# Kernel tuning notes

Hardware: AMD Instinct MI355X
Metric: run time of the kernel (lower is better)

## Reference

```python
import jax, jax.numpy as jnp
import numpy as np

B, T = 64, 4096
CAT_COLS = [0, 1, 2, 3]
VOCABS = [1000, 5000, 200, 50]
EMB_DIMS = [32, 64, 16, 8]
NUM_COLS = list(range(4, 12))  # 8 numeric columns


def setup_inputs() -> dict:
    key = jax.random.key(0)
    ks = jax.random.split(key, 16)
    # numeric part of the dataset
    num = jax.random.normal(ks[0], (B, T, len(NUM_COLS)), dtype=jnp.float32)
    # categorical columns hold raw category ids stored as floats (as in the torch dataset)
    cats = [jax.random.randint(ks[1 + i], (B, T, 1), 0, v).astype(jnp.float32)
            for i, v in enumerate(VOCABS)]
    dataset = jnp.concatenate(cats + [num], axis=-1)  # [B, T, 12]
    inp = {"dataset": dataset}
    for i, (v, d) in enumerate(zip(VOCABS, EMB_DIMS)):
        inp[f"emb{i}"] = jax.random.normal(ks[8 + i], (v, d), dtype=jnp.float32) * 0.02
        # mapping dict {raw_value: contiguous_idx} materialized as a lookup table;
        # unique values are 0..v-1 so the table is the identity permutation
        inp[f"lut{i}"] = jnp.arange(v, dtype=jnp.int32)
    return inp


def reference(dataset, emb0, emb1, emb2, emb3, lut0, lut1, lut2, lut3):
    embs = [emb0, emb1, emb2, emb3]
    luts = [lut0, lut1, lut2, lut3]
    feats = []
    for col, lut, tab in zip(CAT_COLS, luts, embs):
        raw = dataset[:, :, col].astype(jnp.int32)      # [B, T] raw category ids
        mapped = lut[raw]                               # dict remap -> contiguous ids
        feats.append(tab[mapped])                       # [B, T, emb_dim] embedding gather
    feats.append(dataset[:, :, NUM_COLS[0]:NUM_COLS[-1] + 1])  # numeric features [B, T, 8]
    out = jnp.concatenate(feats, axis=-1)               # [B, T, 128]
    return out.reshape(dataset.shape[0], -1, out.shape[-1])
```

## Files before the change

### kernel.cpp

```cpp
#include <hip/hip_runtime.h>
#include <stdint.h>


typedef float f4 __attribute__((ext_vector_type(4)));

__global__ __launch_bounds__(256) void data_embedder_kernel(
    const float* __restrict__ ds,
    const float* __restrict__ e0, const int* __restrict__ l0,
    const float* __restrict__ e1, const int* __restrict__ l1,
    const float* __restrict__ e2, const int* __restrict__ l2,
    const float* __restrict__ e3, const int* __restrict__ l3,
    float* __restrict__ out, int nrows)
{
    int tid  = blockIdx.x * blockDim.x + threadIdx.x;
    int pair = tid >> 5;
    int k    = tid & 31;
    if (pair >= (nrows >> 1)) return;
    int row0 = pair << 1;

    bool s0 = k < 8, s1 = k < 24, s2 = k < 28, s3 = k < 30;
    const float* base = s0 ? e0 : s1 ? e1 : s2 ? e2 : s3 ? e3 : (ds + 4);
    const int*   lut  = s0 ? l0 : s1 ? l1 : s2 ? l2 : l3;
    int stride = s0 ? 32 : s1 ? 64 : s2 ? 16 : s3 ? 8 : 12;
    int off    = (s0 ? k : s1 ? (k - 8) : s2 ? (k - 24) : s3 ? (k - 28) : (k - 30)) * 4;
    int col    = s0 ? 0 : s1 ? 1 : s2 ? 2 : 3;

    const float* drow0 = ds + (size_t)row0 * 12;

    int raw0 = (int)drow0[col];
    int raw1 = (int)drow0[12 + col];
    int m0 = lut[raw0];
    int m1 = lut[raw1];
    int id0 = s3 ? m0 : row0;
    int id1 = s3 ? m1 : row0 + 1;

    f4 v0 = *(const f4*)(base + (size_t)id0 * stride + off);
    f4 v1 = *(const f4*)(base + (size_t)id1 * stride + off);

    float* orow = out + (size_t)row0 * 128 + k * 4;
    *(f4*)(orow)       = v0;
    *(f4*)(orow + 128) = v1;
}

extern "C" void kernel_launch(void* const* d_in, const int* in_sizes, int n_in,
                              void* d_out, int out_size, void* d_ws, size_t ws_size,
                              hipStream_t stream) {
    const float* ds = (const float*)d_in[0];
    const float* e0 = (const float*)d_in[1];
    const int*   l0 = (const int*)  d_in[2];
    const float* e1 = (const float*)d_in[3];
    const int*   l1 = (const int*)  d_in[4];
    const float* e2 = (const float*)d_in[5];
    const int*   l2 = (const int*)  d_in[6];
    const float* e3 = (const float*)d_in[7];
    const int*   l3 = (const int*)  d_in[8];
    float* out = (float*)d_out;

    int nrows = in_sizes[0] / 12;
    long total = (long)(nrows / 2) * 32;
    int block = 256;
    int grid = (int)((total + block - 1) / block);

    data_embedder_kernel<<<grid, block, 0, stream>>>(
        ds, e0, l0, e1, l1, e2, l2, e3, l3, out, nrows);
}
```

Measured before the change: 173.9 us.

## Stage dataset rows and LUT ids in shared memory, 64 rows per block

Each block now loads 64 dataset rows into LDS with coalesced nontemporal vector loads, resolves the four LUT lookups once per row into shared memory, and then has each thread gather and store 8 rows with all loads issued before the stores. This removes the redundant scalar dataset reads and repeated LUT lookups each thread did before, and raises memory-level parallelism per thread. The cost is two block barriers, and the grid size now assumes nrows is a multiple of 64 with no bounds check.

```diff
diff --git a/kernel.cpp b/kernel.cpp
--- a/kernel.cpp
+++ b/kernel.cpp
@@ -3,6 +3,8 @@
 
 
 typedef float f4 __attribute__((ext_vector_type(4)));
+
+#define RPB 64
 
 __global__ __launch_bounds__(256) void data_embedder_kernel(
     const float* __restrict__ ds,
@@ -12,34 +14,52 @@
     const float* __restrict__ e3, const int* __restrict__ l3,
     float* __restrict__ out, int nrows)
 {
-    int tid  = blockIdx.x * blockDim.x + threadIdx.x;
-    int pair = tid >> 5;
-    int k    = tid & 31;
-    if (pair >= (nrows >> 1)) return;
-    int row0 = pair << 1;
+    __shared__ __attribute__((aligned(16))) float sds[RPB * 12];
+    __shared__ int sid[RPB * 4];
+
+    int t = threadIdx.x;
+    int row0 = blockIdx.x * RPB;
+
+    if (t < RPB * 12 / 4) {
+        const f4* src = (const f4*)(ds + (size_t)row0 * 12) + t;
+        f4 v = __builtin_nontemporal_load(src);
+        *(f4*)(sds + t * 4) = v;
+    }
+    __syncthreads();
+
+    {
+        int r = t >> 2, c = t & 3;
+        int raw = (int)sds[r * 12 + c];
+        const int* lut = c == 0 ? l0 : c == 1 ? l1 : c == 2 ? l2 : l3;
+        sid[t] = lut[raw];
+    }
+    __syncthreads();
+
+    int k = t & 31;
+    int g = t >> 5;
 
     bool s0 = k < 8, s1 = k < 24, s2 = k < 28, s3 = k < 30;
     const float* base = s0 ? e0 : s1 ? e1 : s2 ? e2 : s3 ? e3 : (ds + 4);
-    const int*   lut  = s0 ? l0 : s1 ? l1 : s2 ? l2 : l3;
     int stride = s0 ? 32 : s1 ? 64 : s2 ? 16 : s3 ? 8 : 12;
     int off    = (s0 ? k : s1 ? (k - 8) : s2 ? (k - 24) : s3 ? (k - 28) : (k - 30)) * 4;
     int col    = s0 ? 0 : s1 ? 1 : s2 ? 2 : 3;
-
-    const float* drow0 = ds + (size_t)row0 * 12;
-
-    int raw0 = (int)drow0[col];
-    int raw1 = (int)drow0[12 + col];
-    int m0 = lut[raw0];
-    int m1 = lut[raw1];
-    int id0 = s3 ? m0 : row0;
-    int id1 = s3 ? m1 : row0 + 1;
-
-    f4 v0 = *(const f4*)(base + (size_t)id0 * stride + off);
-    f4 v1 = *(const f4*)(base + (size_t)id1 * stride + off);
+    const float* bo = base + off;
 
     float* orow = out + (size_t)row0 * 128 + k * 4;
-    *(f4*)(orow)       = v0;
-    *(f4*)(orow + 128) = v1;
+
+    f4 v[8];
+    #pragma unroll
+    for (int i = 0; i < 8; ++i) {
+        int r  = i * 8 + g;
+        int m  = sid[r * 4 + col];
+        int id = s3 ? m : (row0 + r);
+        v[i] = *(const f4*)(bo + (size_t)id * stride);
+    }
+    #pragma unroll
+    for (int i = 0; i < 8; ++i) {
+        int r = i * 8 + g;
+        *(f4*)(orow + (size_t)r * 128) = v[i];
+    }
 }
 
 extern "C" void kernel_launch(void* const* d_in, const int* in_sizes, int n_in,
@@ -57,10 +77,8 @@
     float* out = (float*)d_out;
 
     int nrows = in_sizes[0] / 12;
-    long total = (long)(nrows / 2) * 32;
-    int block = 256;
-    int grid = (int)((total + block - 1) / block);
+    int grid  = nrows / RPB;
 
-    data_embedder_kernel<<<grid, block, 0, stream>>>(
+    data_embedder_kernel<<<grid, 256, 0, stream>>>(
         ds, e0, l0, e1, l1, e2, l2, e3, l3, out, nrows);
 }
```

After: 172.6 us. About the same (-0.7%).
